# Kernel tuning notes

Measured on AMD Instinct MI355X. Metric: run time of the kernel, lower is better.

Reference implementation:

```python
import jax, jax.numpy as jnp
import numpy as np

B, N, D, H = 2, 2048, 1024, 16
DK = D // H
SCALE = DK ** -0.5


def setup_inputs() -> dict:
    key = jax.random.key(0)
    ks = jax.random.split(key, 11)
    s = D ** -0.5
    return {
        "q": jax.random.normal(ks[0], (B, N, D), jnp.float32),
        "k": jax.random.normal(ks[1], (B, N, D), jnp.float32),
        "v": jax.random.normal(ks[2], (B, N, D), jnp.float32),
        "Wq": jax.random.normal(ks[3], (D, D), jnp.float32) * s,
        "bq": jnp.zeros((D,), jnp.float32),
        "Wk": jax.random.normal(ks[4], (D, D), jnp.float32) * s,
        "bk": jnp.zeros((D,), jnp.float32),
        "Wv": jax.random.normal(ks[5], (D, D), jnp.float32) * s,
        "bv": jnp.zeros((D,), jnp.float32),
        "Wo": jax.random.normal(ks[6], (D, D), jnp.float32) * s,
        "bo": jnp.zeros((D,), jnp.float32),
    }


def _split_heads(x):
    # [b, n, h*d] -> [b, h, n, d]
    b, n, _ = x.shape
    return x.reshape(b, n, H, DK).transpose(0, 2, 1, 3)


def reference(q, k, v, Wq, bq, Wk, bk, Wv, bv, Wo, bo):
    qh = _split_heads(q @ Wq.T + bq)
    kh = _split_heads(k @ Wk.T + bk)
    vh = _split_heads(v @ Wv.T + bv)
    dots = jnp.einsum('bhid,bhjd->bhij', qh, kh) * SCALE
    attn = jax.nn.softmax(dots, axis=-1)
    out = jnp.einsum('bhij,bhjd->bhid', attn, vh)
    out = out.transpose(0, 2, 1, 3).reshape(q.shape[0], q.shape[1], D)
    return out @ Wo.T + bo
```

## Files before the change

kernel.cpp:

```cpp
#include <hip/hip_runtime.h>
#include <hip/hip_bf16.h>
#include <cstdint>
#include <cstddef>

#define BB 2
#define NN 2048
#define DD 1024
#define HH 16
#define DKK 64
#define SCALE 0.125f
#define LOG2E 1.4426950408889634f

typedef __bf16 bf16;
typedef __bf16 bf16x4 __attribute__((ext_vector_type(4)));
typedef __bf16 bf16x8 __attribute__((ext_vector_type(8)));
typedef float f32x4 __attribute__((ext_vector_type(4)));
typedef short s16x4 __attribute__((ext_vector_type(4)));

#define GLD(gp, lp)                                                            \
  __builtin_amdgcn_global_load_lds(                                            \
      (const __attribute__((address_space(1))) void*)(gp),                     \
      (__attribute__((address_space(3))) void*)(lp), 16, 0, 0)

struct CvtArgs { const float* s[7]; bf16* d[7]; int n[7]; };

__global__ void k_cvt(CvtArgs a) {
  const int seg = blockIdx.y;
  const float* __restrict__ s = a.s[seg];
  bf16* __restrict__ d = a.d[seg];
  int i = (blockIdx.x * 256 + threadIdx.x) * 8;
  if (i >= a.n[seg]) return;
  float4 f0 = *(const float4*)(s + i);
  float4 f1 = *(const float4*)(s + i + 4);
  bf16x8 o;
  o[0] = (bf16)f0.x; o[1] = (bf16)f0.y; o[2] = (bf16)f0.z; o[3] = (bf16)f0.w;
  o[4] = (bf16)f1.x; o[5] = (bf16)f1.y; o[6] = (bf16)f1.z; o[7] = (bf16)f1.w;
  *(bf16x8*)(d + i) = o;
}

template <int BN>
__device__ __forceinline__ void gemm_body(
    const bf16* __restrict__ A, const bf16* __restrict__ W,
    const float* __restrict__ bias, bf16* __restrict__ outB,
    float* __restrict__ outF, int mode, float oscale, int m0, int n0) {
  const int K = 1024;
  constexpr int NI = BN / 32;
  constexpr int BI = BN * 8 / 256;
  __shared__ bf16 lA[128 * 64];
  __shared__ bf16 lB[BN * 64];
  const int t = threadIdx.x;
  const int lane = t & 63, quad = lane >> 4, l16 = lane & 15, w = t >> 6;
  const int wm = (w >> 1) * 64, wn = (w & 1) * (BN / 2);

  f32x4 acc[4][NI] = {};

  const bf16* gA[4]; const bf16* gB[BI];
#pragma unroll
  for (int i4 = 0; i4 < 4; i4++) {
    int i = i4 * 256 + t;
    int r = i >> 3, c = (i & 7) ^ (r & 7);
    gA[i4] = A + (size_t)(m0 + r) * K + c * 8;
  }
#pragma unroll
  for (int i4 = 0; i4 < BI; i4++) {
    int i = i4 * 256 + t;
    int r = i >> 3, c = (i & 7) ^ (r & 7);
    gB[i4] = W + (size_t)(n0 + r) * K + c * 8;
  }

  for (int kb = 0; kb < K; kb += 64) {
    __syncthreads();
#pragma unroll
    for (int i4 = 0; i4 < 4; i4++) GLD(gA[i4] + kb, lA + (i4 * 256 + t) * 8);
#pragma unroll
    for (int i4 = 0; i4 < BI; i4++) GLD(gB[i4] + kb, lB + (i4 * 256 + t) * 8);
    __syncthreads();

#pragma unroll
    for (int kb2 = 0; kb2 < 2; kb2++) {
      bf16x8 af[4], bfr[NI];
      const int ch = ((kb2 * 4 + quad) ^ (l16 & 7)) * 8;
#pragma unroll
      for (int i = 0; i < 4; i++)
        af[i] = *(const bf16x8*)(lA + (wm + i * 16 + l16) * 64 + ch);
#pragma unroll
      for (int i = 0; i < NI; i++)
        bfr[i] = *(const bf16x8*)(lB + (wn + i * 16 + l16) * 64 + ch);
#pragma unroll
      for (int mi = 0; mi < 4; mi++)
#pragma unroll
        for (int ni = 0; ni < NI; ni++)
          acc[mi][ni] = __builtin_amdgcn_mfma_f32_16x16x32_bf16(
              af[mi], bfr[ni], acc[mi][ni], 0, 0, 0);
    }
  }

#pragma unroll
  for (int mi = 0; mi < 4; mi++) {
#pragma unroll
    for (int ni = 0; ni < NI; ni++) {
#pragma unroll
      for (int r = 0; r < 4; r++) {
        int gm = m0 + wm + mi * 16 + quad * 4 + r;
        int gn = n0 + wn + ni * 16 + l16;
        float v = (acc[mi][ni][r] + bias[gn]) * oscale;
        if (mode == 3) {
          outF[(size_t)gm * 1024 + gn] = v;
        } else {
          int b = gm >> 11, row = gm & 2047;
          int h = gn >> 6, dk = gn & 63;
          if (mode == 2)
            outB[((size_t)(b * HH + h) * DKK + dk) * NN + row] = (bf16)v;
          else
            outB[((size_t)(b * HH + h) * NN + row) * DKK + dk] = (bf16)v;
        }
      }
    }
  }
}

struct QkvArgs {
  const bf16* A; const bf16* W; const float* b[3]; bf16* o[3]; float sc0;
};

__global__ __launch_bounds__(256, 3) void k_qkv(QkvArgs g) {
  const int z = blockIdx.z;
  gemm_body<128>(g.A + (size_t)z * 4194304, g.W + (size_t)z * 1048576,
                 g.b[z], g.o[z], nullptr, z == 2 ? 2 : 0,
                 z == 0 ? g.sc0 : 1.0f, blockIdx.x * 128, blockIdx.y * 128);
}

__global__ __launch_bounds__(256, 4) void k_oproj(
    const bf16* __restrict__ A, const bf16* __restrict__ W,
    const float* __restrict__ bias, float* __restrict__ out) {
  gemm_body<64>(A, W, bias, nullptr, out, 3, 1.0f, blockIdx.x * 128,
                blockIdx.y * 64);
}

__global__ __launch_bounds__(512, 4) void k_attn(
    const bf16* __restrict__ Qp, const bf16* __restrict__ Kp,
    const bf16* __restrict__ Vt, bf16* __restrict__ Ao) {
  __shared__ bf16 lK[2][128 * 64];
  __shared__ bf16 lV[2][64 * 128];
  const int t = threadIdx.x;
  const int lane = t & 63, quad = lane >> 4, l16 = lane & 15, w = t >> 6;
  const int bh = blockIdx.x;
  const int qt = blockIdx.y;
  const bf16* Qb = Qp + (size_t)bh * NN * DKK;
  const bf16* Kb = Kp + (size_t)bh * NN * DKK;
  const bf16* Vb = Vt + (size_t)bh * DKK * NN;

  const int qr0 = qt * 128 + w * 16;
  bf16x8 qf[2];
#pragma unroll
  for (int kq = 0; kq < 2; kq++)
    qf[kq] = *(const bf16x8*)(Qb + (size_t)(qr0 + l16) * DKK + kq * 32 +
                              quad * 8);

  float lj = 0.f;
  f32x4 oaccT[4] = {};

  const bf16* gK[2]; const bf16* gV[2];
#pragma unroll
  for (int i2 = 0; i2 < 2; i2++) {
    int i = i2 * 512 + t;
    int rK = i >> 3, cK = (i & 7) ^ (rK & 7);
    gK[i2] = Kb + (size_t)rK * DKK + cK * 8;
    int rV = i >> 4, cV = (i & 15) ^ (rV & 15);
    gV[i2] = Vb + (size_t)rV * NN + cV * 8;
  }
  const int swzK0 = (quad ^ (l16 & 7)) * 8;
  const int swzK1 = ((4 + quad) ^ (l16 & 7)) * 8;

#pragma unroll
  for (int i2 = 0; i2 < 2; i2++) {
    GLD(gK[i2], &lK[0][(i2 * 512 + t) * 8]);
    GLD(gV[i2], &lV[0][(i2 * 512 + t) * 8]);
  }

  int p = 0;
  for (int kt = 0; kt < NN; kt += 128) {
    __syncthreads();
    if (kt + 128 < NN) {
#pragma unroll
      for (int i2 = 0; i2 < 2; i2++) {
        GLD(gK[i2] + (size_t)(kt + 128) * DKK, &lK[p ^ 1][(i2 * 512 + t) * 8]);
        GLD(gV[i2] + (kt + 128), &lV[p ^ 1][(i2 * 512 + t) * 8]);
      }
    }

    f32x4 s[8];
#pragma unroll
    for (int tt = 0; tt < 8; tt++) {
      const bf16* kbase = &lK[p][(tt * 16 + l16) * 64];
      bf16x8 kf0 = *(const bf16x8*)(kbase + swzK0);
      bf16x8 kf1 = *(const bf16x8*)(kbase + swzK1);
      f32x4 z = {0.f, 0.f, 0.f, 0.f};
      z = __builtin_amdgcn_mfma_f32_16x16x32_bf16(kf0, qf[0], z, 0, 0, 0);
      z = __builtin_amdgcn_mfma_f32_16x16x32_bf16(kf1, qf[1], z, 0, 0, 0);
      s[tt] = z;
    }

    s16x4 pa[8];
    float rs = 0.f;
#pragma unroll
    for (int tt = 0; tt < 8; tt++) {
      bf16x4 pb;
#pragma unroll
      for (int r = 0; r < 4; r++) {
        float pe = __builtin_amdgcn_exp2f(s[tt][r]);
        rs += pe;
        pb[r] = (bf16)pe;
      }
      pa[tt] = __builtin_bit_cast(s16x4, pb);
    }
    lj += rs;

#pragma unroll
    for (int tt = 0; tt < 8; tt++) {
#pragma unroll
      for (int ni = 0; ni < 4; ni++) {
        int rv = ni * 16 + l16;
        int cc = 2 * tt + (quad >> 1);
        const bf16* vaddr =
            &lV[p][rv * 128 + ((cc ^ l16) * 8) + (quad & 1) * 4];
        s16x4 vb = __builtin_bit_cast(s16x4, *(const bf16x4*)vaddr);
        oaccT[ni] = __builtin_amdgcn_mfma_f32_16x16x16bf16_1k(vb, pa[tt],
                                                              oaccT[ni], 0, 0, 0);
      }
    }
    p ^= 1;
  }

  lj += __shfl_xor(lj, 16);
  lj += __shfl_xor(lj, 32);
  const float inv = 1.0f / lj;
  const int b = bh >> 4, h = bh & 15;
  bf16* dst = Ao + ((size_t)(b * NN) + qr0 + l16) * DD + h * DKK + quad * 4;
#pragma unroll
  for (int ni = 0; ni < 4; ni++) {
    bf16x4 ov;
#pragma unroll
    for (int r = 0; r < 4; r++) ov[r] = (bf16)(oaccT[ni][r] * inv);
    *(bf16x4*)(dst + ni * 16) = ov;
  }
}

extern "C" void kernel_launch(void* const* d_in, const int* in_sizes, int n_in,
                              void* d_out, int out_size, void* d_ws,
                              size_t ws_size, hipStream_t stream) {
  const float* qin = (const float*)d_in[0];
  const float* kin = (const float*)d_in[1];
  const float* vin = (const float*)d_in[2];
  const float* Wq = (const float*)d_in[3];
  const float* bq = (const float*)d_in[4];
  const float* Wk = (const float*)d_in[5];
  const float* bk = (const float*)d_in[6];
  const float* Wv = (const float*)d_in[7];
  const float* bv = (const float*)d_in[8];
  const float* Wo = (const float*)d_in[9];
  const float* bo = (const float*)d_in[10];
  float* out = (float*)d_out;

  const int MN = BB * NN * DD;
  const int WNel = DD * DD;
  bf16* ws = (bf16*)d_ws;
  bf16* Xb = ws;
  bf16* Wb = Xb + 3 * MN;
  bf16* Qp = Wb + 4 * WNel;
  bf16* Kp = Qp + MN;
  bf16* Vt = Kp + MN;
  bf16* Ao = Xb;

  CvtArgs ca{{qin, kin, vin, Wq, Wk, Wv, Wo},
             {Xb, Xb + MN, Xb + 2 * MN, Wb, Wb + WNel, Wb + 2 * WNel,
              Wb + 3 * WNel},
             {MN, MN, MN, WNel, WNel, WNel, WNel}};
  k_cvt<<<dim3(2048, 7), 256, 0, stream>>>(ca);

  QkvArgs g{Xb, Wb, {bq, bk, bv}, {Qp, Kp, Vt}, SCALE * LOG2E};
  k_qkv<<<dim3(32, 8, 3), 256, 0, stream>>>(g);
  k_attn<<<dim3(32, 16), 512, 0, stream>>>(Qp, Kp, Vt, Ao);
  k_oproj<<<dim3(32, 16), 256, 0, stream>>>(Ao, Wb + 3 * WNel, bo, out);
}
```

Before: 224.0 us.

## Split attention key tile across wave halves with 32-row query blocks per wave

Each wave now handles 32 query rows against half of each 128-key tile, instead of 16 query rows against the full tile. Each K and V fragment read from LDS therefore feeds two MFMAs, halving per-wave LDS traffic per unit of compute. The two key-halves' partial outputs and row sums are combined through shared memory at the end. This costs more accumulator registers, which may lower occupancy, plus an extra reduction step with two block barriers.

```diff
diff --git a/kernel.cpp b/kernel.cpp
--- a/kernel.cpp
+++ b/kernel.cpp
@@ -144,21 +144,25 @@
   __shared__ bf16 lV[2][64 * 128];
   const int t = threadIdx.x;
   const int lane = t & 63, quad = lane >> 4, l16 = lane & 15, w = t >> 6;
+  const int wq = w & 3;
+  const int kh = w >> 2;
   const int bh = blockIdx.x;
   const int qt = blockIdx.y;
   const bf16* Qb = Qp + (size_t)bh * NN * DKK;
   const bf16* Kb = Kp + (size_t)bh * NN * DKK;
   const bf16* Vb = Vt + (size_t)bh * DKK * NN;
 
-  const int qr0 = qt * 128 + w * 16;
-  bf16x8 qf[2];
-#pragma unroll
-  for (int kq = 0; kq < 2; kq++)
-    qf[kq] = *(const bf16x8*)(Qb + (size_t)(qr0 + l16) * DKK + kq * 32 +
-                              quad * 8);
-
-  float lj = 0.f;
-  f32x4 oaccT[4] = {};
+  const int qr0 = qt * 128 + wq * 32;
+  bf16x8 qf[2][2];
+#pragma unroll
+  for (int j = 0; j < 2; j++)
+#pragma unroll
+    for (int kq = 0; kq < 2; kq++)
+      qf[j][kq] = *(const bf16x8*)(Qb + (size_t)(qr0 + j * 16 + l16) * DKK +
+                                   kq * 32 + quad * 8);
+
+  float lj[2] = {0.f, 0.f};
+  f32x4 oaccT[2][4] = {};
 
   const bf16* gK[2]; const bf16* gV[2];
 #pragma unroll
@@ -189,60 +193,98 @@
       }
     }
 
-    f32x4 s[8];
-#pragma unroll
-    for (int tt = 0; tt < 8; tt++) {
-      const bf16* kbase = &lK[p][(tt * 16 + l16) * 64];
+    f32x4 s[2][4];
+#pragma unroll
+    for (int tt = 0; tt < 4; tt++) {
+      const bf16* kbase = &lK[p][((kh * 4 + tt) * 16 + l16) * 64];
       bf16x8 kf0 = *(const bf16x8*)(kbase + swzK0);
       bf16x8 kf1 = *(const bf16x8*)(kbase + swzK1);
-      f32x4 z = {0.f, 0.f, 0.f, 0.f};
-      z = __builtin_amdgcn_mfma_f32_16x16x32_bf16(kf0, qf[0], z, 0, 0, 0);
-      z = __builtin_amdgcn_mfma_f32_16x16x32_bf16(kf1, qf[1], z, 0, 0, 0);
-      s[tt] = z;
-    }
-
-    s16x4 pa[8];
-    float rs = 0.f;
-#pragma unroll
-    for (int tt = 0; tt < 8; tt++) {
-      bf16x4 pb;
-#pragma unroll
-      for (int r = 0; r < 4; r++) {
-        float pe = __builtin_amdgcn_exp2f(s[tt][r]);
-        rs += pe;
-        pb[r] = (bf16)pe;
-      }
-      pa[tt] = __builtin_bit_cast(s16x4, pb);
-    }
-    lj += rs;
-
-#pragma unroll
-    for (int tt = 0; tt < 8; tt++) {
+#pragma unroll
+      for (int j = 0; j < 2; j++) {
+        f32x4 z = {0.f, 0.f, 0.f, 0.f};
+        z = __builtin_amdgcn_mfma_f32_16x16x32_bf16(kf0, qf[j][0], z, 0, 0, 0);
+        z = __builtin_amdgcn_mfma_f32_16x16x32_bf16(kf1, qf[j][1], z, 0, 0, 0);
+        s[j][tt] = z;
+      }
+    }
+
+    s16x4 pa[2][4];
+#pragma unroll
+    for (int j = 0; j < 2; j++) {
+      float rs = 0.f;
+#pragma unroll
+      for (int tt = 0; tt < 4; tt++) {
+        bf16x4 pb;
+#pragma unroll
+        for (int r = 0; r < 4; r++) {
+          float pe = __builtin_amdgcn_exp2f(s[j][tt][r]);
+          rs += pe;
+          pb[r] = (bf16)pe;
+        }
+        pa[j][tt] = __builtin_bit_cast(s16x4, pb);
+      }
+      lj[j] += rs;
+    }
+
+#pragma unroll
+    for (int tt = 0; tt < 4; tt++) {
 #pragma unroll
       for (int ni = 0; ni < 4; ni++) {
         int rv = ni * 16 + l16;
-        int cc = 2 * tt + (quad >> 1);
+        int cc = kh * 8 + 2 * tt + (quad >> 1);
         const bf16* vaddr =
             &lV[p][rv * 128 + ((cc ^ l16) * 8) + (quad & 1) * 4];
         s16x4 vb = __builtin_bit_cast(s16x4, *(const bf16x4*)vaddr);
-        oaccT[ni] = __builtin_amdgcn_mfma_f32_16x16x16bf16_1k(vb, pa[tt],
-                                                              oaccT[ni], 0, 0, 0);
+#pragma unroll
+        for (int j = 0; j < 2; j++)
+          oaccT[j][ni] = __builtin_amdgcn_mfma_f32_16x16x16bf16_1k(
+              vb, pa[j][tt], oaccT[j][ni], 0, 0, 0);
       }
     }
     p ^= 1;
   }
 
-  lj += __shfl_xor(lj, 16);
-  lj += __shfl_xor(lj, 32);
-  const float inv = 1.0f / lj;
-  const int b = bh >> 4, h = bh & 15;
-  bf16* dst = Ao + ((size_t)(b * NN) + qr0 + l16) * DD + h * DKK + quad * 4;
-#pragma unroll
-  for (int ni = 0; ni < 4; ni++) {
-    bf16x4 ov;
-#pragma unroll
-    for (int r = 0; r < 4; r++) ov[r] = (bf16)(oaccT[ni][r] * inv);
-    *(bf16x4*)(dst + ni * 16) = ov;
+  __syncthreads();
+  float* redO = (float*)&lK[0][0];
+  float* redL = (float*)&lV[0][0];
+  if (kh == 1) {
+    float* dst = redO + (wq * 64 + lane) * 32;
+#pragma unroll
+    for (int j = 0; j < 2; j++)
+#pragma unroll
+      for (int ni = 0; ni < 4; ni++)
+        *(f32x4*)(dst + (j * 4 + ni) * 4) = oaccT[j][ni];
+    redL[(wq * 64 + lane) * 2 + 0] = lj[0];
+    redL[(wq * 64 + lane) * 2 + 1] = lj[1];
+  }
+  __syncthreads();
+  if (kh == 0) {
+    const float* src = redO + (wq * 64 + lane) * 32;
+#pragma unroll
+    for (int j = 0; j < 2; j++)
+#pragma unroll
+      for (int ni = 0; ni < 4; ni++)
+        oaccT[j][ni] += *(const f32x4*)(src + (j * 4 + ni) * 4);
+    lj[0] += redL[(wq * 64 + lane) * 2 + 0];
+    lj[1] += redL[(wq * 64 + lane) * 2 + 1];
+
+    const int b = bh >> 4, h = bh & 15;
+#pragma unroll
+    for (int j = 0; j < 2; j++) {
+      float l = lj[j];
+      l += __shfl_xor(l, 16);
+      l += __shfl_xor(l, 32);
+      const float inv = 1.0f / l;
+      bf16* dst = Ao + ((size_t)(b * NN) + qr0 + j * 16 + l16) * DD +
+                  h * DKK + quad * 4;
+#pragma unroll
+      for (int ni = 0; ni < 4; ni++) {
+        bf16x4 ov;
+#pragma unroll
+        for (int r = 0; r < 4; r++) ov[r] = (bf16)(oaccT[j][ni][r] * inv);
+        *(bf16x4*)(dst + ni * 16) = ov;
+      }
+    }
   }
 }
 
```

Result: faster. 212.7 us (-5.0%).
